# Optimization experiments

Hardware: AMD Instinct MI355X
Metric: run time of the kernel (lower is better)

## Reference

```python
import jax, jax.numpy as jnp
import numpy as np

N_SAMPLES = 2097152
FEAT_DIM = 16
HIDDEN = 64


def sh_deg4(d):
    # tcnn SphericalHarmonics degree 4 basis (16 outputs).
    # tcnn internally maps input in [0,1] back to [-1,1] via 2*x-1; the module
    # feeds (dirs+1)/2, so the basis is evaluated on the raw (reflected) dirs.
    x, y, z = d[..., 0], d[..., 1], d[..., 2]
    xy, xz, yz = x * y, x * z, y * z
    x2, y2, z2 = x * x, y * y, z * z
    return jnp.stack([
        jnp.full_like(x, 0.28209479177387814),
        -0.48860251190291987 * y,
        0.48860251190291987 * z,
        -0.48860251190291987 * x,
        1.0925484305920792 * xy,
        -1.0925484305920792 * yz,
        0.94617469575755997 * z2 - 0.31539156525251999,
        -1.0925484305920792 * xz,
        0.54627421529603959 * (x2 - y2),
        0.59004358992664352 * y * (-3.0 * x2 + y2),
        2.8906114426405538 * xy * z,
        0.45704579946446572 * y * (1.0 - 5.0 * z2),
        0.3731763325901154 * z * (5.0 * z2 - 3.0),
        0.45704579946446572 * x * (1.0 - 5.0 * z2),
        1.4453057213202769 * z * (x2 - y2),
        0.59004358992664352 * x * (-x2 + 3.0 * y2),
    ], axis=-1)


def _unit(k, shape):
    v = jax.random.normal(k, shape, dtype=jnp.float32)
    return v / jnp.linalg.norm(v, axis=-1, keepdims=True)


def setup_inputs() -> dict:
    key = jax.random.key(0)
    ks = jax.random.split(key, 6)
    in_dim = FEAT_DIM + 16 + 3  # features + SH(deg4) + normals = 35
    return {
        "features": jax.random.normal(ks[0], (N_SAMPLES, FEAT_DIM), dtype=jnp.float32),
        "dirs": _unit(ks[1], (N_SAMPLES, 3)),
        "normals": _unit(ks[2], (N_SAMPLES, 3)),
        "W1": jax.random.normal(ks[3], (in_dim, HIDDEN), dtype=jnp.float32) / np.sqrt(in_dim),
        "W2": jax.random.normal(ks[4], (HIDDEN, HIDDEN), dtype=jnp.float32) / np.sqrt(HIDDEN),
        "W3": jax.random.normal(ks[5], (HIDDEN, 3), dtype=jnp.float32) / np.sqrt(HIDDEN),
    }


def reference(features, dirs, normals, W1, W2, W3):
    # reflect view dirs about the surface normal
    refl = dirs - 2.0 * jnp.sum(dirs * normals, axis=-1, keepdims=True) * normals
    # module does (d+1)/2 then tcnn SH (which undoes it) -> SH on refl directly
    dirs_embd = sh_deg4(refl)
    inp = jnp.concatenate([features, dirs_embd, normals], axis=-1)  # [N, 35]
    h = jax.nn.relu(inp @ W1)
    h = jax.nn.relu(h @ W2)
    color = (h @ W3).astype(jnp.float32)
    return jax.nn.sigmoid(color)  # color_activation = sigmoid
```

## Files before the change

kernel.cpp:

```cpp
#include <hip/hip_runtime.h>
#include <hip/hip_bf16.h>
#include <math.h>

#define NS 2097152
#define NGROUP (NS / 16)
#define NBLOCK 1024
#define NWAVES (NBLOCK * 4)
#define ITERS (NGROUP / NWAVES)

typedef __attribute__((ext_vector_type(8))) short bf16x8;
typedef __attribute__((ext_vector_type(4))) float f32x4;

union FragU { unsigned u[4]; bf16x8 v; };

__device__ __forceinline__ unsigned pkbf16(float lo, float hi) {
    union { __hip_bfloat162 h; unsigned u; } cv;
    cv.h = __halves2bfloat162(__float2bfloat16(lo), __float2bfloat16(hi));
    return cv.u;
}

__global__ __launch_bounds__(256, 4) void radiance_mfma2_kernel(
    const float* __restrict__ features,
    const float* __restrict__ dirs,
    const float* __restrict__ normals,
    const float* __restrict__ W1,
    const float* __restrict__ W2,
    const float* __restrict__ W3,
    float* __restrict__ out)
{
    __shared__ __align__(16) unsigned char lds[4][4096];

    const int tid  = threadIdx.x;
    const int wid  = tid >> 6;
    const int lane = tid & 63;
    const int s    = lane & 15;
    const int hi   = lane >> 4;
    const int wave_id = blockIdx.x * 4 + wid;

    unsigned char* wb  = &lds[wid][0];
    unsigned char* wb2 = wb + 2048;
    const unsigned sw = (unsigned)((s & 7) << 4);

    const f32x4 zero = {0.f, 0.f, 0.f, 0.f};

    unsigned wof[4], rof[2];
    #pragma unroll
    for (int t = 0; t < 4; ++t)
        wof[t] = ((unsigned)(s * 128 + t * 32 + hi * 8)) ^ sw;
    #pragma unroll
    for (int st = 0; st < 2; ++st)
        rof[st] = ((unsigned)(s * 128 + st * 64 + hi * 16)) ^ sw;

    bf16x8 a1[4][2], a2[4][2], a3[2];

    #pragma unroll
    for (int t = 0; t < 4; ++t) {
        #pragma unroll
        for (int st = 0; st < 2; ++st) {
            FragU q;
            #pragma unroll
            for (int d = 0; d < 4; ++d) {
                int k0 = st * 32 + hi * 8 + 2 * d;
                int k1 = k0 + 1;
                int m  = t * 16 + s;
                float w0 = (k0 < 35) ? W1[k0 * 64 + m] : 0.f;
                float w1 = (k1 < 35) ? W1[k1 * 64 + m] : 0.f;
                q.u[d] = pkbf16(w0, w1);
            }
            a1[t][st] = q.v;
        }
    }
    #pragma unroll
    for (int t = 0; t < 4; ++t) {
        #pragma unroll
        for (int st = 0; st < 2; ++st) {
            FragU q;
            #pragma unroll
            for (int d = 0; d < 4; ++d) {
                int k0 = st * 32 + hi * 8 + 2 * d;
                int m  = t * 16 + s;
                q.u[d] = pkbf16(W2[k0 * 64 + m], W2[(k0 + 1) * 64 + m]);
            }
            a2[t][st] = q.v;
        }
    }
    #pragma unroll
    for (int st = 0; st < 2; ++st) {
        FragU q;
        #pragma unroll
        for (int d = 0; d < 4; ++d) {
            int k0 = st * 32 + hi * 8 + 2 * d;
            float w0 = (s < 3) ? W3[k0 * 3 + s] : 0.f;
            float w1 = (s < 3) ? W3[(k0 + 1) * 3 + s] : 0.f;
            q.u[d] = pkbf16(w0, w1);
        }
        a3[st] = q.v;
    }

    float4 cfA, cfB;
    float cdx, cdy, cdz, cnx, cny, cnz;
    {
        unsigned smp = (unsigned)wave_id * 16u + (unsigned)s;
        if (hi < 2) {
            const float* fb = features + (size_t)smp * 16 + hi * 8;
            cfA = *(const float4*)fb;
            cfB = *(const float4*)(fb + 4);
            if (hi == 0) {
                const float* np = normals + (size_t)smp * 3;
                cnx = np[0]; cny = np[1]; cnz = np[2];
            }
        } else {
            const float* dp = dirs + (size_t)smp * 3;
            const float* np = normals + (size_t)smp * 3;
            cdx = dp[0]; cdy = dp[1]; cdz = dp[2];
            cnx = np[0]; cny = np[1]; cnz = np[2];
        }
    }

    unsigned g = (unsigned)wave_id;
    #pragma unroll 1
    for (int it = 0; it < ITERS; ++it) {
        const unsigned gn   = (it == ITERS - 1) ? g : g + (unsigned)NWAVES;
        const unsigned smpn = gn * 16u + (unsigned)s;

        unsigned u0, u1, u2, u3, v0, v1;
        if (hi < 2) {
            u0 = pkbf16(cfA.x, cfA.y); u1 = pkbf16(cfA.z, cfA.w);
            u2 = pkbf16(cfB.x, cfB.y); u3 = pkbf16(cfB.z, cfB.w);
            if (hi == 0) { v0 = pkbf16(cnx, cny); v1 = pkbf16(cnz, 0.f); }
            else         { v0 = 0; v1 = 0; }
            const float* fb = features + (size_t)smpn * 16 + hi * 8;
            cfA = *(const float4*)fb;
            cfB = *(const float4*)(fb + 4);
            if (hi == 0) {
                const float* np = normals + (size_t)smpn * 3;
                cnx = np[0]; cny = np[1]; cnz = np[2];
            }
        } else {
            float dn = cdx * cnx + cdy * cny + cdz * cnz;
            float m2 = -2.0f * dn;
            float x = fmaf(m2, cnx, cdx);
            float y = fmaf(m2, cny, cdy);
            float z = fmaf(m2, cnz, cdz);
            float xy = x * y, xz = x * z, yz = y * z;
            float x2 = x * x, y2 = y * y, z2 = z * z;
            float sh0 = 0.28209479177387814f;
            float sh1 = -0.48860251190291987f * y;
            float sh2 =  0.48860251190291987f * z;
            float sh3 = -0.48860251190291987f * x;
            float sh4 =  1.0925484305920792f * xy;
            float sh5 = -1.0925484305920792f * yz;
            float sh6 = fmaf(0.94617469575755997f, z2, -0.31539156525251999f);
            float sh7 = -1.0925484305920792f * xz;
            float sh8  = 0.54627421529603959f * (x2 - y2);
            float sh9  = 0.59004358992664352f * y * fmaf(-3.0f, x2, y2);
            float sh10 = 2.8906114426405538f * xy * z;
            float sh11 = 0.45704579946446572f * y * fmaf(-5.0f, z2, 1.0f);
            float sh12 = 0.3731763325901154f * z * fmaf(5.0f, z2, -3.0f);
            float sh13 = 0.45704579946446572f * x * fmaf(-5.0f, z2, 1.0f);
            float sh14 = 1.4453057213202769f * z * (x2 - y2);
            float sh15 = 0.59004358992664352f * x * fmaf(-1.0f, x2, 3.0f * y2);
            unsigned e0 = pkbf16(sh0, sh1),  e1 = pkbf16(sh2, sh3);
            unsigned e2 = pkbf16(sh4, sh5),  e3 = pkbf16(sh6, sh7);
            unsigned f0 = pkbf16(sh8, sh9),  f1 = pkbf16(sh10, sh11);
            unsigned f2 = pkbf16(sh12, sh13), f3 = pkbf16(sh14, sh15);
            bool odd = (hi & 1);
            u0 = odd ? f0 : e0; u1 = odd ? f1 : e1;
            u2 = odd ? f2 : e2; u3 = odd ? f3 : e3;
            v0 = 0; v1 = 0;
            const float* dp = dirs + (size_t)smpn * 3;
            const float* np = normals + (size_t)smpn * 3;
            cdx = dp[0]; cdy = dp[1]; cdz = dp[2];
            cnx = np[0]; cny = np[1]; cnz = np[2];
        }
        bf16x8 B0, B1v;
        { FragU q; q.u[0] = u0; q.u[1] = u1; q.u[2] = u2; q.u[3] = u3; B0 = q.v; }
        { FragU q; q.u[0] = v0; q.u[1] = v1; q.u[2] = 0;  q.u[3] = 0;  B1v = q.v; }

        f32x4 acc1[4];
        #pragma unroll
        for (int t = 0; t < 4; ++t)
            acc1[t] = __builtin_amdgcn_mfma_f32_16x16x32_bf16(a1[t][0], B0, zero, 0, 0, 0);
        #pragma unroll
        for (int t = 0; t < 4; ++t)
            acc1[t] = __builtin_amdgcn_mfma_f32_16x16x32_bf16(a1[t][1], B1v, acc1[t], 0, 0, 0);

        #pragma unroll
        for (int t = 0; t < 4; ++t) {
            uint2 w;
            w.x = pkbf16(fmaxf(acc1[t][0], 0.f), fmaxf(acc1[t][1], 0.f));
            w.y = pkbf16(fmaxf(acc1[t][2], 0.f), fmaxf(acc1[t][3], 0.f));
            *(uint2*)(wb + wof[t]) = w;
        }
        bf16x8 hB0 = *(const bf16x8*)(wb + rof[0]);
        bf16x8 hB1 = *(const bf16x8*)(wb + rof[1]);

        f32x4 acc2[4];
        #pragma unroll
        for (int t = 0; t < 4; ++t)
            acc2[t] = __builtin_amdgcn_mfma_f32_16x16x32_bf16(a2[t][0], hB0, zero, 0, 0, 0);
        #pragma unroll
        for (int t = 0; t < 4; ++t)
            acc2[t] = __builtin_amdgcn_mfma_f32_16x16x32_bf16(a2[t][1], hB1, acc2[t], 0, 0, 0);

        #pragma unroll
        for (int t = 0; t < 4; ++t) {
            uint2 w;
            w.x = pkbf16(fmaxf(acc2[t][0], 0.f), fmaxf(acc2[t][1], 0.f));
            w.y = pkbf16(fmaxf(acc2[t][2], 0.f), fmaxf(acc2[t][3], 0.f));
            *(uint2*)(wb2 + wof[t]) = w;
        }
        bf16x8 hC0 = *(const bf16x8*)(wb2 + rof[0]);
        bf16x8 hC1 = *(const bf16x8*)(wb2 + rof[1]);

        f32x4 acc3 = __builtin_amdgcn_mfma_f32_16x16x32_bf16(a3[0], hC0, zero, 0, 0, 0);
        acc3 = __builtin_amdgcn_mfma_f32_16x16x32_bf16(a3[1], hC1, acc3, 0, 0, 0);

        float o0 = __fdividef(1.0f, 1.0f + __expf(-acc3[0]));
        float o1 = __fdividef(1.0f, 1.0f + __expf(-acc3[1]));
        float o2 = __fdividef(1.0f, 1.0f + __expf(-acc3[2]));
        if (hi == 0) {
            float* ob = out + (size_t)(g * 16u + (unsigned)s) * 3;
            ob[0] = o0; ob[1] = o1; ob[2] = o2;
        }
        g = gn;
    }
}

extern "C" void kernel_launch(void* const* d_in, const int* in_sizes, int n_in,
                              void* d_out, int out_size, void* d_ws, size_t ws_size,
                              hipStream_t stream) {
    const float* features = (const float*)d_in[0];
    const float* dirs     = (const float*)d_in[1];
    const float* normals  = (const float*)d_in[2];
    const float* W1       = (const float*)d_in[3];
    const float* W2       = (const float*)d_in[4];
    const float* W3       = (const float*)d_in[5];
    float* out = (float*)d_out;

    radiance_mfma2_kernel<<<NBLOCK, 256, 0, stream>>>(
        features, dirs, normals, W1, W2, W3, out);
}
```

Baseline: 314.3 us.

## Permute hidden-dim K ordering to keep MFMA outputs in registers, dropping LDS round-trips

The rows of W2 and W3 are permuted so that each MFMA accumulator layout directly matches the next layer's B-operand fragment layout. Hidden activations are then packed into bf16 fragments in registers rather than written to and read back from LDS. W3 rows are placed so each lane produces a single output channel, and the final store becomes one coalesced scalar per lane. This removes the LDS traffic and waits between layers, at the cost of more complex weight indexing and a correctness dependence on the permutation matching the MFMA lane mapping.

```diff
diff --git a/kernel.cpp b/kernel.cpp
--- a/kernel.cpp
+++ b/kernel.cpp
@@ -19,7 +19,12 @@
     return cv.u;
 }
 
-__global__ __launch_bounds__(256, 4) void radiance_mfma2_kernel(
+__device__ __forceinline__ int permk(int p) {
+    int st = p >> 5, hi = (p >> 3) & 3, j = p & 7;
+    return (st * 2 + (j >> 2)) * 16 + hi * 4 + (j & 3);
+}
+
+__global__ __launch_bounds__(256, 4) void radiance_mfma4_kernel(
     const float* __restrict__ features,
     const float* __restrict__ dirs,
     const float* __restrict__ normals,
@@ -28,8 +33,6 @@
     const float* __restrict__ W3,
     float* __restrict__ out)
 {
-    __shared__ __align__(16) unsigned char lds[4][4096];
-
     const int tid  = threadIdx.x;
     const int wid  = tid >> 6;
     const int lane = tid & 63;
@@ -37,22 +40,9 @@
     const int hi   = lane >> 4;
     const int wave_id = blockIdx.x * 4 + wid;
 
-    unsigned char* wb  = &lds[wid][0];
-    unsigned char* wb2 = wb + 2048;
-    const unsigned sw = (unsigned)((s & 7) << 4);
-
     const f32x4 zero = {0.f, 0.f, 0.f, 0.f};
 
-    unsigned wof[4], rof[2];
-    #pragma unroll
-    for (int t = 0; t < 4; ++t)
-        wof[t] = ((unsigned)(s * 128 + t * 32 + hi * 8)) ^ sw;
-    #pragma unroll
-    for (int st = 0; st < 2; ++st)
-        rof[st] = ((unsigned)(s * 128 + st * 64 + hi * 16)) ^ sw;
-
     bf16x8 a1[4][2], a2[4][2], a3[2];
-
     #pragma unroll
     for (int t = 0; t < 4; ++t) {
         #pragma unroll
@@ -77,24 +67,30 @@
             FragU q;
             #pragma unroll
             for (int d = 0; d < 4; ++d) {
-                int k0 = st * 32 + hi * 8 + 2 * d;
+                int p0 = st * 32 + hi * 8 + 2 * d;
+                int n0 = permk(p0), n1 = permk(p0 + 1);
                 int m  = t * 16 + s;
-                q.u[d] = pkbf16(W2[k0 * 64 + m], W2[(k0 + 1) * 64 + m]);
+                q.u[d] = pkbf16(W2[n0 * 64 + m], W2[n1 * 64 + m]);
             }
             a2[t][st] = q.v;
         }
     }
-    #pragma unroll
-    for (int st = 0; st < 2; ++st) {
-        FragU q;
-        #pragma unroll
-        for (int d = 0; d < 4; ++d) {
-            int k0 = st * 32 + hi * 8 + 2 * d;
-            float w0 = (s < 3) ? W3[k0 * 3 + s] : 0.f;
-            float w1 = (s < 3) ? W3[(k0 + 1) * 3 + s] : 0.f;
-            q.u[d] = pkbf16(w0, w1);
-        }
-        a3[st] = q.v;
+    {
+        bool live = ((s & 3) == 0) && (s < 12);
+        int ch = s >> 2;
+        #pragma unroll
+        for (int st = 0; st < 2; ++st) {
+            FragU q;
+            #pragma unroll
+            for (int d = 0; d < 4; ++d) {
+                int p0 = st * 32 + hi * 8 + 2 * d;
+                int n0 = permk(p0), n1 = permk(p0 + 1);
+                float w0 = live ? W3[n0 * 3 + ch] : 0.f;
+                float w1 = live ? W3[n1 * 3 + ch] : 0.f;
+                q.u[d] = pkbf16(w0, w1);
+            }
+            a3[st] = q.v;
+        }
     }
 
     float4 cfA, cfB;
@@ -185,43 +181,42 @@
         for (int t = 0; t < 4; ++t)
             acc1[t] = __builtin_amdgcn_mfma_f32_16x16x32_bf16(a1[t][1], B1v, acc1[t], 0, 0, 0);
 
-        #pragma unroll
-        for (int t = 0; t < 4; ++t) {
-            uint2 w;
-            w.x = pkbf16(fmaxf(acc1[t][0], 0.f), fmaxf(acc1[t][1], 0.f));
-            w.y = pkbf16(fmaxf(acc1[t][2], 0.f), fmaxf(acc1[t][3], 0.f));
-            *(uint2*)(wb + wof[t]) = w;
-        }
-        bf16x8 hB0 = *(const bf16x8*)(wb + rof[0]);
-        bf16x8 hB1 = *(const bf16x8*)(wb + rof[1]);
+        bf16x8 B2[2];
+        #pragma unroll
+        for (int st = 0; st < 2; ++st) {
+            FragU q;
+            q.u[0] = pkbf16(fmaxf(acc1[st*2][0],   0.f), fmaxf(acc1[st*2][1],   0.f));
+            q.u[1] = pkbf16(fmaxf(acc1[st*2][2],   0.f), fmaxf(acc1[st*2][3],   0.f));
+            q.u[2] = pkbf16(fmaxf(acc1[st*2+1][0], 0.f), fmaxf(acc1[st*2+1][1], 0.f));
+            q.u[3] = pkbf16(fmaxf(acc1[st*2+1][2], 0.f), fmaxf(acc1[st*2+1][3], 0.f));
+            B2[st] = q.v;
+        }
 
         f32x4 acc2[4];
         #pragma unroll
         for (int t = 0; t < 4; ++t)
-            acc2[t] = __builtin_amdgcn_mfma_f32_16x16x32_bf16(a2[t][0], hB0, zero, 0, 0, 0);
-        #pragma unroll
-        for (int t = 0; t < 4; ++t)
-            acc2[t] = __builtin_amdgcn_mfma_f32_16x16x32_bf16(a2[t][1], hB1, acc2[t], 0, 0, 0);
-
-        #pragma unroll
-        for (int t = 0; t < 4; ++t) {
-            uint2 w;
-            w.x = pkbf16(fmaxf(acc2[t][0], 0.f), fmaxf(acc2[t][1], 0.f));
-            w.y = pkbf16(fmaxf(acc2[t][2], 0.f), fmaxf(acc2[t][3], 0.f));
-            *(uint2*)(wb2 + wof[t]) = w;
-        }
-        bf16x8 hC0 = *(const bf16x8*)(wb2 + rof[0]);
-        bf16x8 hC1 = *(const bf16x8*)(wb2 + rof[1]);
-
-        f32x4 acc3 = __builtin_amdgcn_mfma_f32_16x16x32_bf16(a3[0], hC0, zero, 0, 0, 0);
-        acc3 = __builtin_amdgcn_mfma_f32_16x16x32_bf16(a3[1], hC1, acc3, 0, 0, 0);
-
-        float o0 = __fdividef(1.0f, 1.0f + __expf(-acc3[0]));
-        float o1 = __fdividef(1.0f, 1.0f + __expf(-acc3[1]));
-        float o2 = __fdividef(1.0f, 1.0f + __expf(-acc3[2]));
-        if (hi == 0) {
-            float* ob = out + (size_t)(g * 16u + (unsigned)s) * 3;
-            ob[0] = o0; ob[1] = o1; ob[2] = o2;
+            acc2[t] = __builtin_amdgcn_mfma_f32_16x16x32_bf16(a2[t][0], B2[0], zero, 0, 0, 0);
+        #pragma unroll
+        for (int t = 0; t < 4; ++t)
+            acc2[t] = __builtin_amdgcn_mfma_f32_16x16x32_bf16(a2[t][1], B2[1], acc2[t], 0, 0, 0);
+
+        bf16x8 B3[2];
+        #pragma unroll
+        for (int st = 0; st < 2; ++st) {
+            FragU q;
+            q.u[0] = pkbf16(fmaxf(acc2[st*2][0],   0.f), fmaxf(acc2[st*2][1],   0.f));
+            q.u[1] = pkbf16(fmaxf(acc2[st*2][2],   0.f), fmaxf(acc2[st*2][3],   0.f));
+            q.u[2] = pkbf16(fmaxf(acc2[st*2+1][0], 0.f), fmaxf(acc2[st*2+1][1], 0.f));
+            q.u[3] = pkbf16(fmaxf(acc2[st*2+1][2], 0.f), fmaxf(acc2[st*2+1][3], 0.f));
+            B3[st] = q.v;
+        }
+
+        f32x4 acc3 = __builtin_amdgcn_mfma_f32_16x16x32_bf16(a3[0], B3[0], zero, 0, 0, 0);
+        acc3 = __builtin_amdgcn_mfma_f32_16x16x32_bf16(a3[1], B3[1], acc3, 0, 0, 0);
+
+        float o = __fdividef(1.0f, 1.0f + __expf(-acc3[0]));
+        if (hi < 3) {
+            out[(size_t)g * 48 + (unsigned)s * 3 + (unsigned)hi] = o;
         }
         g = gn;
     }
@@ -238,6 +233,6 @@
     const float* W3       = (const float*)d_in[5];
     float* out = (float*)d_out;
 
-    radiance_mfma2_kernel<<<NBLOCK, 256, 0, stream>>>(
+    radiance_mfma4_kernel<<<NBLOCK, 256, 0, stream>>>(
         features, dirs, normals, W1, W2, W3, out);
 }
```

Measured after the change: 290.3 us. -7.7%, faster.
